# Kernel tuning notes

Hardware: AMD Instinct MI355X
Metric: run time of the kernel (lower is better)

Reference implementation:

```python
import jax, jax.numpy as jnp
import numpy as np

T, N, F, H, C = 32, 20000, 128, 128, 10
LN_EPS = 1e-5


def setup_inputs() -> dict:
    key = jax.random.key(0)
    ks = jax.random.split(key, 11)
    u = lambda k, shp, bound: jax.random.uniform(k, shp, jnp.float32, -bound, bound)
    bh = 1.0 / np.sqrt(H)  # torch RNNCell / Linear init scale
    return {
        "X": jax.random.normal(ks[0], (T, N, F), jnp.float32),
        "W_ih": u(ks[1], (H, F), bh),
        "W_hh": u(ks[2], (H, H), bh),
        "b_ih": u(ks[3], (H,), bh),
        "b_hh": u(ks[4], (H,), bh),
        "ln_gamma": jnp.ones((H,), jnp.float32),
        "ln_beta": jnp.zeros((H,), jnp.float32),
        "attn_W": u(ks[5], (1, H), bh),
        "attn_b": u(ks[6], (1,), bh),
        "dense_W": u(ks[7], (C, H), bh),
        "dense_b": u(ks[8], (C,), bh),
    }


def reference(X, W_ih, W_hh, b_ih, b_hh, ln_gamma, ln_beta, attn_W, attn_b, dense_W, dense_b):
    # --- R: initial hidden (no ReLU, as in source init branch) ---
    h0 = X[0] @ W_ih.T + b_hh + b_ih  # (N, H)

    def step(h, x):
        h_new = jax.nn.relu(x @ W_ih.T + b_ih + h @ W_hh.T + b_hh)
        return h_new, h_new

    _, outs = jax.lax.scan(step, h0, X)  # (T, N, H)

    # LayerNorm over last dim (dropout is identity in eval / p=0)
    mu = jnp.mean(outs, axis=-1, keepdims=True)
    var = jnp.var(outs, axis=-1, keepdims=True)
    outs = (outs - mu) * jax.lax.rsqrt(var + LN_EPS) * ln_gamma + ln_beta

    # --- attn: linear -> softmax over time axis 0 ---
    a = jax.nn.softmax(outs @ attn_W.T + attn_b, axis=0)  # (T, N, 1)

    # --- dense: linear -> weight by attention -> sum over time ---
    d = outs @ dense_W.T + dense_b  # (T, N, C)
    return jnp.sum(d * a, axis=0)  # (N, C)
```

## Files before the change

### kernel.cpp

```cpp
#include <hip/hip_runtime.h>
#include <math.h>

#define TT 32
#define NN 20000
#define FF 128
#define HH 128
#define CC 10
#define RPB 32
#define NTHREADS 512

typedef __attribute__((ext_vector_type(8))) _Float16 f16x8;
typedef __attribute__((ext_vector_type(4))) _Float16 f16x4;
typedef __attribute__((ext_vector_type(4))) float f32x4;

#define PLANE_LO 16384
#define SMW_OFF  32768
#define WSTRIDE  2064
#define Y_OFF    98816
#define A_ADDR(row, chunk) (((row) << 9) + ((((chunk) ^ ((row) & 15))) << 4))
#define Y_ADDR(row, chunk) (Y_OFF + ((row) << 8) + ((((chunk) ^ ((row) & 15))) << 4))

__device__ __forceinline__ void split8(float4 a, float4 b, f16x8* hi, f16x8* lo) {
    float v[8] = {a.x, a.y, a.z, a.w, b.x, b.y, b.z, b.w};
    f16x8 h, l;
#pragma unroll
    for (int j = 0; j < 8; ++j) {
        _Float16 hh = (_Float16)v[j];
        h[j] = hh;
        l[j] = (_Float16)(v[j] - (float)hh);
    }
    *hi = h; *lo = l;
}

__global__ __launch_bounds__(NTHREADS, 1)
void grn8(const float* __restrict__ X,
          const float* __restrict__ W_ih,
          const float* __restrict__ W_hh,
          const float* __restrict__ b_ih,
          const float* __restrict__ b_hh,
          const float* __restrict__ gamma,
          const float* __restrict__ beta,
          const float* __restrict__ attn_w,
          const float* __restrict__ dense_W,
          const float* __restrict__ dense_b,
          float* __restrict__ out)
{
    __shared__ __align__(16) char smem[107008];
    char* smA = smem;

    const int tid  = threadIdx.x;
    const int lane = tid & 63;
    const int wave = tid >> 6;
    const int n0   = blockIdx.x * RPB;

    for (int jj = tid; jj < 4096; jj += NTHREADS) {
        const int kg = jj >> 7;
        const int c  = jj & 127;
        const int k0 = kg << 3;
        const float* src = (k0 < 128) ? (W_ih + c * 128 + k0)
                                      : (W_hh + c * 128 + (k0 - 128));
        float4 w0 = *(const float4*)src;
        float4 w1 = *(const float4*)(src + 4);
        f16x8 w;
        w[0]=(_Float16)w0.x; w[1]=(_Float16)w0.y; w[2]=(_Float16)w0.z; w[3]=(_Float16)w0.w;
        w[4]=(_Float16)w1.x; w[5]=(_Float16)w1.y; w[6]=(_Float16)w1.z; w[7]=(_Float16)w1.w;
        *(f16x8*)(smem + SMW_OFF + kg * WSTRIDE + c * 16) = w;
    }

    f16x8 wd[4];
    {
        const int c = lane & 15;
#pragma unroll
        for (int ks = 0; ks < 4; ++ks) {
            f16x8 pk;
#pragma unroll
            for (int j = 0; j < 8; ++j) {
                const int k = ks * 32 + ((lane >> 4) << 3) + j;
                float v = 0.f;
                if (c < 10)       v = dense_W[c * 128 + k];
                else if (c == 10) v = attn_w[k];
                pk[j] = (_Float16)v;
            }
            wd[ks] = pk;
        }
    }

    const int c0 = (wave << 4) + ((lane >> 4) << 2);
    f32x4 bias4;
    {
        float4 bi = *(const float4*)(b_ih + c0);
        float4 bh = *(const float4*)(b_hh + c0);
        bias4[0] = bi.x + bh.x; bias4[1] = bi.y + bh.y;
        bias4[2] = bi.z + bh.z; bias4[3] = bi.w + bh.w;
    }
    const int kch   = 16 + (c0 >> 3);
    const int c0off = (c0 & 4) << 1;

    const int lrow = tid >> 4;
    const int lc   = tid & 15;
    float g[8], bb[8];
    {
        const int cb = lc << 3;
        float4 g0 = *(const float4*)(gamma + cb);
        float4 g1 = *(const float4*)(gamma + cb + 4);
        float4 b0 = *(const float4*)(beta  + cb);
        float4 b1 = *(const float4*)(beta  + cb + 4);
        g[0]=g0.x; g[1]=g0.y; g[2]=g0.z; g[3]=g0.w;
        g[4]=g1.x; g[5]=g1.y; g[6]=g1.z; g[7]=g1.w;
        bb[0]=b0.x; bb[1]=b0.y; bb[2]=b0.z; bb[3]=b0.w;
        bb[4]=b1.x; bb[5]=b1.y; bb[6]=b1.z; bb[7]=b1.w;
    }

    {
        const float* xs0 = X + (size_t)(n0 + lrow) * FF + (lc << 3);
        float4 p0 = *(const float4*)xs0;
        float4 p1 = *(const float4*)(xs0 + 4);
        f16x8 hi, lo;
        split8(p0, p1, &hi, &lo);
        *(f16x8*)(smA + A_ADDR(lrow, lc)) = hi;
        *(f16x8*)(smA + PLANE_LO + A_ADDR(lrow, lc)) = lo;
        f16x8 z;
#pragma unroll
        for (int j = 0; j < 8; ++j) z[j] = (_Float16)0.f;
        for (int i = tid; i < 1024; i += NTHREADS) {
            const int pl  = i >> 9;
            const int row = (i >> 4) & 31;
            const int ch  = 16 + (i & 15);
            *(f16x8*)(smA + pl * PLANE_LO + (row << 9) + (ch << 4)) = z;
        }
    }
    __syncthreads();

    {
        f32x4 acc[2];
        acc[0] = (f32x4){0.f,0.f,0.f,0.f};
        acc[1] = (f32x4){0.f,0.f,0.f,0.f};
#pragma unroll
        for (int ks = 0; ks < 8; ++ks) {
            const int kc = (ks << 2) + (lane >> 4);
            f16x8 a0h = *(const f16x8*)(smA + A_ADDR(lane & 15, kc));
            f16x8 a0l = *(const f16x8*)(smA + PLANE_LO + A_ADDR(lane & 15, kc));
            f16x8 a1h = *(const f16x8*)(smA + A_ADDR(16 + (lane & 15), kc));
            f16x8 a1l = *(const f16x8*)(smA + PLANE_LO + A_ADDR(16 + (lane & 15), kc));
            f16x8 b0 = *(const f16x8*)(smem + SMW_OFF + kc * WSTRIDE
                                       + (((wave << 4) + (lane & 15)) << 4));
            acc[0] = __builtin_amdgcn_mfma_f32_16x16x32_f16(b0, a0h, acc[0], 0, 0, 0);
            acc[0] = __builtin_amdgcn_mfma_f32_16x16x32_f16(b0, a0l, acc[0], 0, 0, 0);
            acc[1] = __builtin_amdgcn_mfma_f32_16x16x32_f16(b0, a1h, acc[1], 0, 0, 0);
            acc[1] = __builtin_amdgcn_mfma_f32_16x16x32_f16(b0, a1l, acc[1], 0, 0, 0);
        }
        __syncthreads();
#pragma unroll
        for (int mt = 0; mt < 2; ++mt) {
            const int row = (lane & 15) + (mt << 4);
            f16x4 hi4, lo4;
#pragma unroll
            for (int q = 0; q < 4; ++q) {
                const float v = acc[mt][q] + bias4[q];
                _Float16 hh = (_Float16)v;
                hi4[q] = hh;
                lo4[q] = (_Float16)(v - (float)hh);
            }
            const int addr = (row << 9) + (((kch ^ (row & 15))) << 4) + c0off;
            *(f16x4*)(smA + addr) = hi4;
            *(f16x4*)(smA + PLANE_LO + addr) = lo4;
        }
    }
    __syncthreads();

    float stm[4], stz[4], sta[4];
#pragma unroll
    for (int s = 0; s < 4; ++s) { stm[s] = -INFINITY; stz[s] = 0.f; sta[s] = 0.f; }

    for (int t = 0; t < TT; ++t) {
        float4 p0, p1;
        if (t < TT - 1) {
            const float* xs0 = X + ((size_t)(t + 1) * NN + n0 + lrow) * FF + (lc << 3);
            p0 = *(const float4*)xs0;
            p1 = *(const float4*)(xs0 + 4);
        }

        f32x4 acc[2];
        acc[0] = (f32x4){0.f,0.f,0.f,0.f};
        acc[1] = (f32x4){0.f,0.f,0.f,0.f};
#pragma unroll
        for (int ks = 0; ks < 8; ++ks) {
            const int kc = (ks << 2) + (lane >> 4);
            f16x8 a0h = *(const f16x8*)(smA + A_ADDR(lane & 15, kc));
            f16x8 a0l = *(const f16x8*)(smA + PLANE_LO + A_ADDR(lane & 15, kc));
            f16x8 a1h = *(const f16x8*)(smA + A_ADDR(16 + (lane & 15), kc));
            f16x8 a1l = *(const f16x8*)(smA + PLANE_LO + A_ADDR(16 + (lane & 15), kc));
            f16x8 b0 = *(const f16x8*)(smem + SMW_OFF + kc * WSTRIDE
                                       + (((wave << 4) + (lane & 15)) << 4));
            acc[0] = __builtin_amdgcn_mfma_f32_16x16x32_f16(b0, a0h, acc[0], 0, 0, 0);
            acc[0] = __builtin_amdgcn_mfma_f32_16x16x32_f16(b0, a0l, acc[0], 0, 0, 0);
            acc[1] = __builtin_amdgcn_mfma_f32_16x16x32_f16(b0, a1h, acc[1], 0, 0, 0);
            acc[1] = __builtin_amdgcn_mfma_f32_16x16x32_f16(b0, a1l, acc[1], 0, 0, 0);
        }
        __syncthreads();

#pragma unroll
        for (int mt = 0; mt < 2; ++mt) {
            const int row = (lane & 15) + (mt << 4);
            f16x4 hi4, lo4;
#pragma unroll
            for (int q = 0; q < 4; ++q) {
                const float v = fmaxf(acc[mt][q] + bias4[q], 0.f);
                _Float16 hh = (_Float16)v;
                hi4[q] = hh;
                lo4[q] = (_Float16)(v - (float)hh);
            }
            const int addr = (row << 9) + (((kch ^ (row & 15))) << 4) + c0off;
            *(f16x4*)(smA + addr) = hi4;
            *(f16x4*)(smA + PLANE_LO + addr) = lo4;
        }
        if (t < TT - 1) {
            f16x8 hi, lo;
            split8(p0, p1, &hi, &lo);
            *(f16x8*)(smA + A_ADDR(lrow, lc)) = hi;
            *(f16x8*)(smA + PLANE_LO + A_ADDR(lrow, lc)) = lo;
        }
        __syncthreads();

        {
            f16x8 hv = *(const f16x8*)(smA + A_ADDR(lrow, 16 + lc));
            float v[8];
            float s1 = 0.f, s2 = 0.f;
#pragma unroll
            for (int j = 0; j < 8; ++j) { v[j] = (float)hv[j]; }
#pragma unroll
            for (int j = 0; j < 8; ++j) { s1 += v[j]; s2 += v[j] * v[j]; }
            s1 += __shfl_xor(s1, 1); s2 += __shfl_xor(s2, 1);
            s1 += __shfl_xor(s1, 2); s2 += __shfl_xor(s2, 2);
            s1 += __shfl_xor(s1, 4); s2 += __shfl_xor(s2, 4);
            s1 += __shfl_xor(s1, 8); s2 += __shfl_xor(s2, 8);
            const float mu  = s1 * (1.f / 128.f);
            const float var = s2 * (1.f / 128.f) - mu * mu;
            const float rsi = rsqrtf(var + 1e-5f);
            f16x8 y;
#pragma unroll
            for (int j = 0; j < 8; ++j)
                y[j] = (_Float16)((v[j] - mu) * rsi * g[j] + bb[j]);
            *(f16x8*)(smem + Y_ADDR(lrow, lc)) = y;
        }
        __syncthreads();

        if (wave < 2) {
            f32x4 acc2 = (f32x4){0.f,0.f,0.f,0.f};
#pragma unroll
            for (int ks = 0; ks < 4; ++ks) {
                const int kc = (ks << 2) + (lane >> 4);
                f16x8 a = *(const f16x8*)(smem + Y_ADDR((wave << 4) + (lane & 15), kc));
                acc2 = __builtin_amdgcn_mfma_f32_16x16x32_f16(a, wd[ks], acc2, 0, 0, 0);
            }
#pragma unroll
            for (int r = 0; r < 4; ++r) {
                const float dval = acc2[r];
                const float lg = __shfl(dval, (lane & 48) + 10);
                const float mn = fmaxf(stm[r], lg);
                const float sc = __expf(stm[r] - mn);
                const float e  = __expf(lg - mn);
                stz[r] = stz[r] * sc + e;
                sta[r] = sta[r] * sc + e * dval;
                stm[r] = mn;
            }
        }
    }

    if (wave < 2) {
        const int c = lane & 15;
        if (c < CC) {
            const float db = dense_b[c];
#pragma unroll
            for (int r = 0; r < 4; ++r) {
                const int row = (wave << 4) + ((lane >> 4) << 2) + r;
                out[(size_t)(n0 + row) * CC + c] = sta[r] / stz[r] + db;
            }
        }
    }
}

extern "C" void kernel_launch(void* const* d_in, const int* in_sizes, int n_in,
                              void* d_out, int out_size, void* d_ws, size_t ws_size,
                              hipStream_t stream) {
    const float* X      = (const float*)d_in[0];
    const float* W_ih   = (const float*)d_in[1];
    const float* W_hh   = (const float*)d_in[2];
    const float* b_ih   = (const float*)d_in[3];
    const float* b_hh   = (const float*)d_in[4];
    const float* gamma  = (const float*)d_in[5];
    const float* beta   = (const float*)d_in[6];
    const float* attn_w = (const float*)d_in[7];
    const float* dW     = (const float*)d_in[9];
    const float* db     = (const float*)d_in[10];
    float* out = (float*)d_out;
    (void)in_sizes; (void)n_in; (void)out_size; (void)d_ws; (void)ws_size;

    grn8<<<dim3(NN / RPB), dim3(NTHREADS), 0, stream>>>(
        X, W_ih, W_hh, b_ih, b_hh, gamma, beta, attn_w, dW, db, out);
}
```

Before: 217.8 us.

## Precompute fp16 weights in prep kernel and hold recurrent weights in registers

A small prep kernel converts W_ih/W_hh and the dense/attention weights to fp16 once, in the workspace. The main kernel then loads its per-wave weight fragments straight into registers instead of staging them in LDS, so LDS use drops from about 107KB to 40KB. This removes per-block weight conversion and the LDS B-operand loads inside the time loop. In exchange it adds register pressure, a second kernel launch, and a dependence on workspace size.

```diff
diff --git a/kernel.cpp b/kernel.cpp
--- a/kernel.cpp
+++ b/kernel.cpp
@@ -14,9 +14,7 @@
 typedef __attribute__((ext_vector_type(4))) float f32x4;
 
 #define PLANE_LO 16384
-#define SMW_OFF  32768
-#define WSTRIDE  2064
-#define Y_OFF    98816
+#define Y_OFF    32768
 #define A_ADDR(row, chunk) (((row) << 9) + ((((chunk) ^ ((row) & 15))) << 4))
 #define Y_ADDR(row, chunk) (Y_OFF + ((row) << 8) + ((((chunk) ^ ((row) & 15))) << 4))
 
@@ -32,20 +30,53 @@
     *hi = h; *lo = l;
 }
 
+__global__ __launch_bounds__(256, 1)
+void grn_prep(const float* __restrict__ W_ih,
+              const float* __restrict__ W_hh,
+              const float* __restrict__ dense_W,
+              const float* __restrict__ attn_w,
+              _Float16* __restrict__ wsg)
+{
+    const int i  = blockIdx.x * 256 + threadIdx.x;
+    const int kg = i & 31;
+    const int c  = i >> 5;
+    const int k0 = kg << 3;
+    const float* src = (k0 < 128) ? (W_ih + c * 128 + k0)
+                                  : (W_hh + c * 128 + (k0 - 128));
+    float4 w0 = *(const float4*)src;
+    float4 w1 = *(const float4*)(src + 4);
+    f16x8 w;
+    w[0]=(_Float16)w0.x; w[1]=(_Float16)w0.y; w[2]=(_Float16)w0.z; w[3]=(_Float16)w0.w;
+    w[4]=(_Float16)w1.x; w[5]=(_Float16)w1.y; w[6]=(_Float16)w1.z; w[7]=(_Float16)w1.w;
+    *(f16x8*)(wsg + kg * 1024 + c * 8) = w;
+
+    if (i < 256) {
+        const int kg2 = i >> 4;
+        const int cc  = i & 15;
+        f16x8 d;
+#pragma unroll
+        for (int j = 0; j < 8; ++j) {
+            const int k = (kg2 << 3) + j;
+            float v = 0.f;
+            if (cc < 10)       v = dense_W[cc * 128 + k];
+            else if (cc == 10) v = attn_w[k];
+            d[j] = (_Float16)v;
+        }
+        *(f16x8*)(wsg + 32768 + kg2 * 128 + cc * 8) = d;
+    }
+}
+
 __global__ __launch_bounds__(NTHREADS, 1)
-void grn8(const float* __restrict__ X,
-          const float* __restrict__ W_ih,
-          const float* __restrict__ W_hh,
-          const float* __restrict__ b_ih,
-          const float* __restrict__ b_hh,
-          const float* __restrict__ gamma,
-          const float* __restrict__ beta,
-          const float* __restrict__ attn_w,
-          const float* __restrict__ dense_W,
-          const float* __restrict__ dense_b,
-          float* __restrict__ out)
+void grn_r8(const float* __restrict__ X,
+            const _Float16* __restrict__ wsg,
+            const float* __restrict__ b_ih,
+            const float* __restrict__ b_hh,
+            const float* __restrict__ gamma,
+            const float* __restrict__ beta,
+            const float* __restrict__ dense_b,
+            float* __restrict__ out)
 {
-    __shared__ __align__(16) char smem[107008];
+    __shared__ __align__(16) char smem[40960];
     char* smA = smem;
 
     const int tid  = threadIdx.x;
@@ -53,35 +84,23 @@
     const int wave = tid >> 6;
     const int n0   = blockIdx.x * RPB;
 
-    for (int jj = tid; jj < 4096; jj += NTHREADS) {
-        const int kg = jj >> 7;
-        const int c  = jj & 127;
-        const int k0 = kg << 3;
-        const float* src = (k0 < 128) ? (W_ih + c * 128 + k0)
-                                      : (W_hh + c * 128 + (k0 - 128));
-        float4 w0 = *(const float4*)src;
-        float4 w1 = *(const float4*)(src + 4);
-        f16x8 w;
-        w[0]=(_Float16)w0.x; w[1]=(_Float16)w0.y; w[2]=(_Float16)w0.z; w[3]=(_Float16)w0.w;
-        w[4]=(_Float16)w1.x; w[5]=(_Float16)w1.y; w[6]=(_Float16)w1.z; w[7]=(_Float16)w1.w;
-        *(f16x8*)(smem + SMW_OFF + kg * WSTRIDE + c * 16) = w;
+    f16x8 Wf[8];
+    {
+        const int c = (wave << 4) + (lane & 15);
+#pragma unroll
+        for (int ks = 0; ks < 8; ++ks) {
+            const int kc = (ks << 2) + (lane >> 4);
+            Wf[ks] = *(const f16x8*)(wsg + kc * 1024 + c * 8);
+        }
     }
 
     f16x8 wd[4];
     {
-        const int c = lane & 15;
+        const int cc = lane & 15;
 #pragma unroll
         for (int ks = 0; ks < 4; ++ks) {
-            f16x8 pk;
-#pragma unroll
-            for (int j = 0; j < 8; ++j) {
-                const int k = ks * 32 + ((lane >> 4) << 3) + j;
-                float v = 0.f;
-                if (c < 10)       v = dense_W[c * 128 + k];
-                else if (c == 10) v = attn_w[k];
-                pk[j] = (_Float16)v;
-            }
-            wd[ks] = pk;
+            const int kc = (ks << 2) + (lane >> 4);
+            wd[ks] = *(const f16x8*)(wsg + 32768 + kc * 128 + cc * 8);
         }
     }
 
@@ -142,12 +161,10 @@
             f16x8 a0l = *(const f16x8*)(smA + PLANE_LO + A_ADDR(lane & 15, kc));
             f16x8 a1h = *(const f16x8*)(smA + A_ADDR(16 + (lane & 15), kc));
             f16x8 a1l = *(const f16x8*)(smA + PLANE_LO + A_ADDR(16 + (lane & 15), kc));
-            f16x8 b0 = *(const f16x8*)(smem + SMW_OFF + kc * WSTRIDE
-                                       + (((wave << 4) + (lane & 15)) << 4));
-            acc[0] = __builtin_amdgcn_mfma_f32_16x16x32_f16(b0, a0h, acc[0], 0, 0, 0);
-            acc[0] = __builtin_amdgcn_mfma_f32_16x16x32_f16(b0, a0l, acc[0], 0, 0, 0);
-            acc[1] = __builtin_amdgcn_mfma_f32_16x16x32_f16(b0, a1h, acc[1], 0, 0, 0);
-            acc[1] = __builtin_amdgcn_mfma_f32_16x16x32_f16(b0, a1l, acc[1], 0, 0, 0);
+            acc[0] = __builtin_amdgcn_mfma_f32_16x16x32_f16(Wf[ks], a0h, acc[0], 0, 0, 0);
+            acc[0] = __builtin_amdgcn_mfma_f32_16x16x32_f16(Wf[ks], a0l, acc[0], 0, 0, 0);
+            acc[1] = __builtin_amdgcn_mfma_f32_16x16x32_f16(Wf[ks], a1h, acc[1], 0, 0, 0);
+            acc[1] = __builtin_amdgcn_mfma_f32_16x16x32_f16(Wf[ks], a1l, acc[1], 0, 0, 0);
         }
         __syncthreads();
 #pragma unroll
@@ -190,12 +207,10 @@
             f16x8 a0l = *(const f16x8*)(smA + PLANE_LO + A_ADDR(lane & 15, kc));
             f16x8 a1h = *(const f16x8*)(smA + A_ADDR(16 + (lane & 15), kc));
             f16x8 a1l = *(const f16x8*)(smA + PLANE_LO + A_ADDR(16 + (lane & 15), kc));
-            f16x8 b0 = *(const f16x8*)(smem + SMW_OFF + kc * WSTRIDE
-                                       + (((wave << 4) + (lane & 15)) << 4));
-            acc[0] = __builtin_amdgcn_mfma_f32_16x16x32_f16(b0, a0h, acc[0], 0, 0, 0);
-            acc[0] = __builtin_amdgcn_mfma_f32_16x16x32_f16(b0, a0l, acc[0], 0, 0, 0);
-            acc[1] = __builtin_amdgcn_mfma_f32_16x16x32_f16(b0, a1h, acc[1], 0, 0, 0);
-            acc[1] = __builtin_amdgcn_mfma_f32_16x16x32_f16(b0, a1l, acc[1], 0, 0, 0);
+            acc[0] = __builtin_amdgcn_mfma_f32_16x16x32_f16(Wf[ks], a0h, acc[0], 0, 0, 0);
+            acc[0] = __builtin_amdgcn_mfma_f32_16x16x32_f16(Wf[ks], a0l, acc[0], 0, 0, 0);
+            acc[1] = __builtin_amdgcn_mfma_f32_16x16x32_f16(Wf[ks], a1h, acc[1], 0, 0, 0);
+            acc[1] = __builtin_amdgcn_mfma_f32_16x16x32_f16(Wf[ks], a1l, acc[1], 0, 0, 0);
         }
         __syncthreads();
 
@@ -294,8 +309,10 @@
     const float* dW     = (const float*)d_in[9];
     const float* db     = (const float*)d_in[10];
     float* out = (float*)d_out;
-    (void)in_sizes; (void)n_in; (void)out_size; (void)d_ws; (void)ws_size;
-
-    grn8<<<dim3(NN / RPB), dim3(NTHREADS), 0, stream>>>(
-        X, W_ih, W_hh, b_ih, b_hh, gamma, beta, attn_w, dW, db, out);
+    _Float16* wsg = (_Float16*)d_ws;
+    (void)in_sizes; (void)n_in; (void)out_size; (void)ws_size;
+
+    grn_prep<<<dim3(16), dim3(256), 0, stream>>>(W_ih, W_hh, dW, attn_w, wsg);
+    grn_r8<<<dim3(NN / RPB), dim3(NTHREADS), 0, stream>>>(
+        X, wsg, b_ih, b_hh, gamma, beta, db, out);
 }
```

After: 200.5 us. 7.9% less time.
